# Kernel tuning notes

Measured on AMD Instinct MI355X. Metric: run time of the kernel, lower is better.

Reference implementation:

```python
import jax, jax.numpy as jnp
import numpy as np

R_EPOCHS = 150
R_LR = 0.1
LMDA = 0.005


def setup_inputs() -> dict:
    key = jax.random.key(0)
    k_img, k_u = jax.random.split(key)
    B, K, M2 = 2048, 1024, 1024  # batch, neurons, M**2 pixels
    img = jax.random.normal(k_img, (B, M2), dtype=jnp.float32)
    U = jax.random.normal(k_u, (K, M2), dtype=jnp.float32)
    U = U / jnp.linalg.norm(U, axis=1, keepdims=True)  # F.normalize(U, dim=1)
    return {"img": img, "U": U}


def _soft_threshold(x, alpha):
    # relu(x - a) - relu(-x - a) == sign(x) * max(|x| - a, 0)
    return jnp.sign(x) * jnp.maximum(jnp.abs(x) - alpha, 0.0)


def reference(img, U):
    B = img.shape[0]
    K = U.shape[0]

    def step(R, _):
        # dL/dR for L = sum((img - R @ U)**2)  ->  2 * (R @ U - img) @ U.T
        grad = 2.0 * ((R @ U - img) @ U.T)
        R = _soft_threshold(R - R_LR * grad, LMDA)
        return R, None

    R0 = jnp.zeros((B, K), dtype=img.dtype)
    R, _ = jax.lax.scan(step, R0, None, length=R_EPOCHS)
    # In torch, R is updated via .data / no_grad, so it is a leaf w.r.t. autograd
    R = jax.lax.stop_gradient(R)
    return R @ U
```

## Files before the change

kernel.cpp:

```cpp
#include <hip/hip_runtime.h>
#include <cstddef>
#include <cstdint>

using f32x4  = __attribute__((ext_vector_type(4))) float;
using bf16x8 = __attribute__((ext_vector_type(8))) short;
using u16x4  = __attribute__((ext_vector_type(4))) unsigned short;
using u32x4  = __attribute__((ext_vector_type(4))) unsigned int;
typedef unsigned short u16;
typedef unsigned int   u32;

#define LMDA 0.005f

__device__ __forceinline__ u16 f2bf(float f) {
    union { float f; uint32_t u; } v; v.f = f;
    return (u16)((v.u + 0x7FFFu + ((v.u >> 16) & 1u)) >> 16);
}
__device__ __forceinline__ float bf2f(u16 b) {
    union { uint32_t u; float f; } v; v.u = ((uint32_t)b) << 16;
    return v.f;
}
__device__ __forceinline__ float bits2f(u32 u) {
    union { uint32_t u; float f; } v; v.u = u;
    return v.f;
}
__device__ __forceinline__ void split2(float x, u16& h, u16& l) {
    h = f2bf(x); l = f2bf(x - bf2f(h));
}
__device__ __forceinline__ float sthr(float x) {
    float ax = fabsf(x) - LMDA;
    return ax > 0.0f ? copysignf(ax, x) : 0.0f;
}

__device__ __forceinline__ void gload16(const u16* g, u16* l) {
    __builtin_amdgcn_global_load_lds(
        (const __attribute__((address_space(1))) unsigned int*)(const void*)g,
        (__attribute__((address_space(3))) unsigned int*)(void*)l, 16, 0, 0);
}

__global__ __launch_bounds__(512, 2)
void pc_step(const u16* __restrict__ Rh, const u16* __restrict__ Rl,
             const u16* __restrict__ Woh, const u32* __restrict__ Cp,
             u16* __restrict__ Nh, u16* __restrict__ Nl)
{
    __shared__ __align__(16) u16 S[3][24 * 512];

    const int fid = blockIdx.x;
    const int sid = (fid & 7) * 32 + (fid >> 3);
    const int tr = sid >> 3;
    const int tc = sid & 7;
    const int row0 = tr << 6;
    const int col0 = tc << 7;

    const int tid  = threadIdx.x;
    const int lane = tid & 63;
    const int w    = tid >> 6;
    const int mr   = w >> 2;
    const int nc   = w & 3;
    const int l15  = lane & 15;
    const int lg   = lane >> 4;
    const int l8   = lane << 3;

    const u16* gsrc[3];
    int loff[3];
    #pragma unroll
    for (int t = 0; t < 3; ++t) {
        const int c = w * 3 + t;
        const u16* base;
        int r, kh;
        if (c < 8) {
            kh = (c >> 2) & 1;
            base = Rh;
            r = row0 + ((c & 3) << 4) + l15;
        } else {
            const int cb = c - 8;
            kh = cb >> 3;
            base = Woh;
            r = col0 + ((cb & 7) << 4) + l15;
        }
        gsrc[t] = base + ((size_t)r << 10) + (kh << 5) + (lg << 3);
        loff[t] = (c << 9) + l8;
    }
    auto stage = [&](int b, int k) {
        #pragma unroll
        for (int t = 0; t < 3; ++t)
            gload16(gsrc[t] + k, &S[b][loff[t]]);
    };

    f32x4 acc[2][2] = {};

    stage(0, 0);
    stage(1, 64);

    for (int s = 0; s < 16; ++s) {
        if (s < 15) asm volatile("s_waitcnt vmcnt(3)" ::: "memory");
        else        asm volatile("s_waitcnt vmcnt(0)" ::: "memory");
        __builtin_amdgcn_s_barrier();
        asm volatile("" ::: "memory");
        if (s + 2 < 16) {
            int nb = s + 2; nb -= (nb >= 3) ? 3 : 0; nb -= (nb >= 3) ? 3 : 0;
            nb = (s + 2) % 3;
            stage(nb, (s + 2) << 6);
        }

        const u16* Sb = S[s % 3];
        bf16x8 rh[2][2], wo[2][2];
        #pragma unroll
        for (int kh = 0; kh < 2; ++kh) {
            #pragma unroll
            for (int mf = 0; mf < 2; ++mf) {
                const int g = (mr << 1) + mf;
                rh[mf][kh] = *(const bf16x8*)&Sb[(((kh << 2) + g) << 9) + l8];
            }
            #pragma unroll
            for (int nf = 0; nf < 2; ++nf) {
                const int g = (nc << 1) + nf;
                wo[nf][kh] = *(const bf16x8*)&Sb[((8 + (kh << 3) + g) << 9) + l8];
            }
        }
        #pragma unroll
        for (int kh = 0; kh < 2; ++kh)
            #pragma unroll
            for (int mf = 0; mf < 2; ++mf)
                #pragma unroll
                for (int nf = 0; nf < 2; ++nf)
                    acc[mf][nf] = __builtin_amdgcn_mfma_f32_16x16x32_bf16(
                        wo[nf][kh], rh[mf][kh], acc[mf][nf], 0, 0, 0);
        asm volatile("" ::: "memory");
    }

    #pragma unroll
    for (int mf = 0; mf < 2; ++mf) {
        #pragma unroll
        for (int nf = 0; nf < 2; ++nf) {
            const int m  = row0 + (mr << 5) + (mf << 4) + l15;
            const int n0 = col0 + (nc << 5) + (nf << 4) + (lg << 2);
            const size_t idx = ((size_t)m << 10) + n0;
            const u16x4 rh4 = *(const u16x4*)&Rh[idx];
            const u16x4 rl4 = *(const u16x4*)&Rl[idx];
            const u32x4 cp4 = *(const u32x4*)&Cp[idx];
            u16x4 hv, lv;
            #pragma unroll
            for (int e = 0; e < 4; ++e) {
                const float cs = bits2f(cp4[e] & 0xFFFF0000u) + bits2f(cp4[e] << 16);
                float r = bf2f(rh4[e]) + bf2f(rl4[e]);
                float x = acc[mf][nf][e] + 0.8f * r + cs;
                u16 hh, ll; split2(sthr(x), hh, ll);
                hv[e] = hh; lv[e] = ll;
            }
            *(u16x4*)&Nh[idx] = hv;
            *(u16x4*)&Nl[idx] = lv;
        }
    }
}

__global__ __launch_bounds__(512, 2)
void gemm_fin(const u16* __restrict__ Rh, const u16* __restrict__ Rl,
              const u16* __restrict__ Bm, float* __restrict__ OutF)
{
    constexpr int NCH = 32;
    __shared__ __align__(16) u16 S[2][NCH * 512];

    const int fid = blockIdx.x;
    const int sid = (fid & 7) * 32 + (fid >> 3);
    const int tr = sid >> 3;
    const int tc = sid & 7;
    const int row0 = tr << 6;
    const int col0 = tc << 7;

    const int tid  = threadIdx.x;
    const int lane = tid & 63;
    const int w    = tid >> 6;
    const int mr   = w >> 2;
    const int nc   = w & 3;
    const int l15  = lane & 15;
    const int lg   = lane >> 4;
    const int l8   = lane << 3;

    const u16* gsrc[4];
    int loff[4];
    #pragma unroll
    for (int t = 0; t < 4; ++t) {
        const int c = (w << 2) + t;
        const u16* base;
        int r, kh;
        if (c < 16) {
            const int h = c >> 3;
            kh = (c >> 2) & 1;
            base = h ? Rl : Rh;
            r = row0 + ((c & 3) << 4) + l15;
        } else {
            const int cb = c - 16;
            kh = cb >> 3;
            base = Bm;
            r = col0 + ((cb & 7) << 4) + l15;
        }
        gsrc[t] = base + ((size_t)r << 10) + (kh << 5) + (lg << 3);
        loff[t] = (c << 9) + l8;
    }
    auto stage = [&](int b, int k) {
        #pragma unroll
        for (int t = 0; t < 4; ++t)
            gload16(gsrc[t] + k, &S[b][loff[t]]);
    };

    f32x4 acc[2][2] = {};

    stage(0, 0);

    for (int s = 0; s < 16; ++s) {
        asm volatile("s_waitcnt vmcnt(0)" ::: "memory");
        __builtin_amdgcn_s_barrier();
        asm volatile("" ::: "memory");
        if (s < 15) stage((s + 1) & 1, (s + 1) << 6);

        const u16* Sb = S[s & 1];
        bf16x8 rh[2][2], rl[2][2], wo[2][2];
        #pragma unroll
        for (int kh = 0; kh < 2; ++kh) {
            #pragma unroll
            for (int mf = 0; mf < 2; ++mf) {
                const int g = (mr << 1) + mf;
                rh[mf][kh] = *(const bf16x8*)&Sb[(((kh << 2) + g) << 9) + l8];
                rl[mf][kh] = *(const bf16x8*)&Sb[((8 + (kh << 2) + g) << 9) + l8];
            }
            #pragma unroll
            for (int nf = 0; nf < 2; ++nf) {
                const int g = (nc << 1) + nf;
                wo[nf][kh] = *(const bf16x8*)&Sb[((16 + (kh << 3) + g) << 9) + l8];
            }
        }
        #pragma unroll
        for (int kh = 0; kh < 2; ++kh)
            #pragma unroll
            for (int mf = 0; mf < 2; ++mf)
                #pragma unroll
                for (int nf = 0; nf < 2; ++nf) {
                    acc[mf][nf] = __builtin_amdgcn_mfma_f32_16x16x32_bf16(
                        wo[nf][kh], rh[mf][kh], acc[mf][nf], 0, 0, 0);
                    acc[mf][nf] = __builtin_amdgcn_mfma_f32_16x16x32_bf16(
                        wo[nf][kh], rl[mf][kh], acc[mf][nf], 0, 0, 0);
                }
        asm volatile("" ::: "memory");
    }

    #pragma unroll
    for (int mf = 0; mf < 2; ++mf)
        #pragma unroll
        for (int nf = 0; nf < 2; ++nf) {
            const int m  = row0 + (mr << 5) + (mf << 4) + l15;
            const int n0 = col0 + (nc << 5) + (nf << 4) + (lg << 2);
            *(f32x4*)&OutF[((size_t)m << 10) + n0] = acc[mf][nf];
        }
}

template<int EPI>
__global__ __launch_bounds__(512, 2)
void gemm_ista(const u16* __restrict__ Ah, const u16* __restrict__ Al,
               const u16* __restrict__ Bh, const u16* __restrict__ Bl,
               int Nt,
               u32* __restrict__ OutP,
               u16* __restrict__ OutH, u16* __restrict__ OutL)
{
    __shared__ __align__(16) u16 S[3][48 * 512];

    const int nwg = gridDim.x;
    const int fid = blockIdx.x;
    const int sid = (fid & 7) * (nwg >> 3) + (fid >> 3);
    const int row0 = (sid / Nt) << 7;
    const int col0 = (sid % Nt) << 6;

    const int tid  = threadIdx.x;
    const int lane = tid & 63;
    const int w    = tid >> 6;
    const int mr = w >> 2, nc = (w >> 1) & 1, ks = w & 1;

    const u16* gb[6];
    int cf[6];
    #pragma unroll
    for (int t = 0; t < 6; ++t) {
        const int c = w * 6 + t;
        const u16* base; int r; int kss;
        if (c < 32) {
            const int h = (c >> 4) & 1; kss = (c >> 3) & 1;
            base = h ? Al : Ah;
            r = row0 + ((c & 7) << 4) + (lane & 15);
        } else {
            const int cb = c - 32;
            const int h = (cb >> 3) & 1; kss = (cb >> 2) & 1;
            base = h ? Bl : Bh;
            r = col0 + ((cb & 3) << 4) + (lane & 15);
        }
        gb[t] = base + ((size_t)r << 10) + (kss << 5) + ((lane >> 4) << 3);
        cf[t] = c << 9;
    }
    auto stage = [&](int b, int koff) {
        #pragma unroll
        for (int t = 0; t < 6; ++t)
            gload16(gb[t] + koff, &S[b][cf[t]]);
    };

    f32x4 acc[4][2] = {};

    stage(0, 0);
    stage(1, 64);

    #pragma unroll
    for (int s = 0; s < 16; ++s) {
        if (s <= 14) asm volatile("s_waitcnt vmcnt(6)" ::: "memory");
        else         asm volatile("s_waitcnt vmcnt(0)" ::: "memory");
        __builtin_amdgcn_s_barrier();
        asm volatile("" ::: "memory");
        if (s + 2 < 16) stage((s + 2) % 3, (s + 2) << 6);

        const u16* Sb = S[s % 3];
        const int ab = (ks << 3) + (mr << 2);
        const int bb = 32 + (ks << 2) + (nc << 1);
        bf16x8 ah[4], al[4], bh[2], bl[2];
        #pragma unroll
        for (int i = 0; i < 4; ++i) {
            ah[i] = *(const bf16x8*)&Sb[(ab + i)      * 512 + (lane << 3)];
            al[i] = *(const bf16x8*)&Sb[(ab + 16 + i) * 512 + (lane << 3)];
        }
        #pragma unroll
        for (int j = 0; j < 2; ++j) {
            bh[j] = *(const bf16x8*)&Sb[(bb + j)     * 512 + (lane << 3)];
            bl[j] = *(const bf16x8*)&Sb[(bb + 8 + j) * 512 + (lane << 3)];
        }
        #pragma unroll
        for (int i = 0; i < 4; ++i)
            #pragma unroll
            for (int j = 0; j < 2; ++j)
                acc[i][j] = __builtin_amdgcn_mfma_f32_16x16x32_bf16(ah[i], bh[j], acc[i][j], 0, 0, 0);
        #pragma unroll
        for (int i = 0; i < 4; ++i)
            #pragma unroll
            for (int j = 0; j < 2; ++j)
                acc[i][j] = __builtin_amdgcn_mfma_f32_16x16x32_bf16(al[i], bh[j], acc[i][j], 0, 0, 0);
        #pragma unroll
        for (int i = 0; i < 4; ++i)
            #pragma unroll
            for (int j = 0; j < 2; ++j)
                acc[i][j] = __builtin_amdgcn_mfma_f32_16x16x32_bf16(ah[i], bl[j], acc[i][j], 0, 0, 0);
        asm volatile("" ::: "memory");
    }

    __syncthreads();
    f32x4* red = (f32x4*)&S[0][0];
    const int wquad = (mr << 1) + nc;
    #pragma unroll
    for (int ih = 0; ih < 2; ++ih) {
        #pragma unroll
        for (int j = 0; j < 2; ++j) {
            const int isrc = ks ? ih : (2 + ih);
            const int slot = ((((wquad << 1) | ks) << 2) | (ih << 1) | j);
            red[slot * 64 + lane] = acc[isrc][j];
        }
    }
    __syncthreads();

    const int gr0 = row0 + (mr << 6) + ((lane >> 4) << 2);
    const int gc  = col0 + (nc << 5) + (lane & 15);
    #pragma unroll
    for (int ih = 0; ih < 2; ++ih) {
        #pragma unroll
        for (int j = 0; j < 2; ++j) {
            const int i    = ks ? (2 + ih) : ih;
            const int slot = ((((wquad << 1) | (ks ^ 1)) << 2) | (ih << 1) | j);
            f32x4 sum = acc[i][j] + red[slot * 64 + lane];
            #pragma unroll
            for (int e = 0; e < 4; ++e) {
                const int grow = gr0 + (i << 4) + e;
                const int gcol = gc + (j << 4);
                const size_t idx = ((size_t)grow << 10) + gcol;
                const float p = sum[e];
                if (EPI == 1) {
                    float f = 0.2f * p;
                    u16 ch, cl; split2(f, ch, cl);
                    OutP[idx] = (((u32)ch) << 16) | (u32)cl;
                    u16 h, l; split2(sthr(f), h, l);
                    OutH[idx] = h; OutL[idx] = l;
                } else {
                    float x = (grow == gcol) ? 0.0f : -0.2f * p;
                    OutH[idx] = f2bf(x);
                }
            }
        }
    }
}

__global__ void k_split(const float* __restrict__ in, u16* __restrict__ hi,
                        u16* __restrict__ lo, int n)
{
    int i = blockIdx.x * 256 + threadIdx.x;
    if (i < n) { u16 h, l; split2(in[i], h, l); hi[i] = h; lo[i] = l; }
}

__global__ __launch_bounds__(256)
void k_transpose_split(const float* __restrict__ in, u16* __restrict__ hi,
                       u16* __restrict__ lo)
{
    __shared__ float t[32][33];
    const int bx = blockIdx.x, by = blockIdx.y;
    const int lx = threadIdx.x & 31, ly = threadIdx.x >> 5;
    #pragma unroll
    for (int rr = 0; rr < 4; ++rr) {
        int r = ly * 4 + rr;
        t[r][lx] = in[(size_t)(by * 32 + r) * 1024 + bx * 32 + lx];
    }
    __syncthreads();
    #pragma unroll
    for (int rr = 0; rr < 4; ++rr) {
        int r = ly * 4 + rr;
        u16 h, l; split2(t[lx][r], h, l);
        size_t idx = (size_t)(bx * 32 + r) * 1024 + by * 32 + lx;
        hi[idx] = h; lo[idx] = l;
    }
}

extern "C" void kernel_launch(void* const* d_in, const int* in_sizes, int n_in,
                              void* d_out, int out_size, void* d_ws, size_t ws_size,
                              hipStream_t stream) {
    const float* img = (const float*)d_in[0];
    const float* U   = (const float*)d_in[1];
    float* out = (float*)d_out;

    char* ws = (char*)d_ws;
    auto MB = [](size_t m) { return m << 20; };
    u16*   Uh  = (u16*)(ws + MB(0));
    u16*   Ul  = (u16*)(ws + MB(2));
    u16*   Uth = (u16*)(ws + MB(4));
    u16*   Utl = (u16*)(ws + MB(6));
    u16*   Woh = (u16*)(ws + MB(8));
    u32*   Cp  = (u32*)(ws + MB(12));
    u16*   Rah = (u16*)(ws + MB(20));
    u16*   Ral = (u16*)(ws + MB(24));
    u16*   Rbh = (u16*)(ws + MB(28));
    u16*   Rbl = (u16*)(ws + MB(32));
    u16*   Ih  = Rbh;
    u16*   Il  = Rbl;

    k_split<<<4096, 256, 0, stream>>>(U, Uh, Ul, 1024 * 1024);
    k_split<<<8192, 256, 0, stream>>>(img, Ih, Il, 2048 * 1024);
    k_transpose_split<<<dim3(32, 32), 256, 0, stream>>>(U, Uth, Utl);

    gemm_ista<4><<<128, 512, 0, stream>>>(Uh, Ul, Uh, Ul, 16,
                                          nullptr, Woh, nullptr);
    gemm_ista<1><<<256, 512, 0, stream>>>(Ih, Il, Uh, Ul, 16,
                                          Cp, Rah, Ral);

    u16 *ch = Rah, *cl = Ral, *nh = Rbh, *nl = Rbl;
    for (int it = 0; it < 149; ++it) {
        pc_step<<<256, 512, 0, stream>>>(ch, cl, Woh, Cp, nh, nl);
        u16* t;
        t = ch; ch = nh; nh = t;
        t = cl; cl = nl; nl = t;
    }

    gemm_fin<<<256, 512, 0, stream>>>(ch, cl, Uth, out);
}
```

Measured before the change: 2.691 ms.

## Restructure pc_step to 4-wave blocks with 32-wide K stages and 2x4 MFMA tiles

The per-iteration ISTA step kernel drops from 8 to 4 waves per block. Each wave now computes a 32x64 output sub-tile (2x4 MFMA fragments) instead of 32x32, and the K loop runs 32 stages of 32 instead of 16 stages of 64. Shared memory per block halves, so more blocks can be resident. The intent is to raise register-level reuse of the loaded fragments and improve occupancy. In exchange there are twice as many barriers and pipeline stages per tile, and fewer waves share each block's loads.

```diff
diff --git a/kernel.cpp b/kernel.cpp
--- a/kernel.cpp
+++ b/kernel.cpp
@@ -37,12 +37,12 @@
         (__attribute__((address_space(3))) unsigned int*)(void*)l, 16, 0, 0);
 }
 
-__global__ __launch_bounds__(512, 2)
+__global__ __launch_bounds__(256, 4)
 void pc_step(const u16* __restrict__ Rh, const u16* __restrict__ Rl,
              const u16* __restrict__ Woh, const u32* __restrict__ Cp,
              u16* __restrict__ Nh, u16* __restrict__ Nl)
 {
-    __shared__ __align__(16) u16 S[3][24 * 512];
+    __shared__ __align__(16) u16 S[3][12 * 512];
 
     const int fid = blockIdx.x;
     const int sid = (fid & 7) * 32 + (fid >> 3);
@@ -54,8 +54,8 @@
     const int tid  = threadIdx.x;
     const int lane = tid & 63;
     const int w    = tid >> 6;
-    const int mr   = w >> 2;
-    const int nc   = w & 3;
+    const int mr   = w >> 1;
+    const int nc   = w & 1;
     const int l15  = lane & 15;
     const int lg   = lane >> 4;
     const int l8   = lane << 3;
@@ -66,18 +66,10 @@
     for (int t = 0; t < 3; ++t) {
         const int c = w * 3 + t;
         const u16* base;
-        int r, kh;
-        if (c < 8) {
-            kh = (c >> 2) & 1;
-            base = Rh;
-            r = row0 + ((c & 3) << 4) + l15;
-        } else {
-            const int cb = c - 8;
-            kh = cb >> 3;
-            base = Woh;
-            r = col0 + ((cb & 7) << 4) + l15;
-        }
-        gsrc[t] = base + ((size_t)r << 10) + (kh << 5) + (lg << 3);
+        int r;
+        if (c < 4) { base = Rh;  r = row0 + ((c & 3) << 4) + l15; }
+        else       { base = Woh; r = col0 + ((c - 4) << 4) + l15; }
+        gsrc[t] = base + ((size_t)r << 10) + (lg << 3);
         loff[t] = (c << 9) + l8;
     }
     auto stage = [&](int b, int k) {
@@ -86,54 +78,41 @@
             gload16(gsrc[t] + k, &S[b][loff[t]]);
     };
 
-    f32x4 acc[2][2] = {};
+    f32x4 acc[2][4] = {};
 
     stage(0, 0);
-    stage(1, 64);
-
-    for (int s = 0; s < 16; ++s) {
-        if (s < 15) asm volatile("s_waitcnt vmcnt(3)" ::: "memory");
+    stage(1, 32);
+
+    for (int s = 0; s < 32; ++s) {
+        if (s < 31) asm volatile("s_waitcnt vmcnt(3)" ::: "memory");
         else        asm volatile("s_waitcnt vmcnt(0)" ::: "memory");
         __builtin_amdgcn_s_barrier();
         asm volatile("" ::: "memory");
-        if (s + 2 < 16) {
-            int nb = s + 2; nb -= (nb >= 3) ? 3 : 0; nb -= (nb >= 3) ? 3 : 0;
-            nb = (s + 2) % 3;
-            stage(nb, (s + 2) << 6);
-        }
+        if (s + 2 < 32) stage((s + 2) % 3, (s + 2) << 5);
 
         const u16* Sb = S[s % 3];
-        bf16x8 rh[2][2], wo[2][2];
-        #pragma unroll
-        for (int kh = 0; kh < 2; ++kh) {
-            #pragma unroll
-            for (int mf = 0; mf < 2; ++mf) {
-                const int g = (mr << 1) + mf;
-                rh[mf][kh] = *(const bf16x8*)&Sb[(((kh << 2) + g) << 9) + l8];
-            }
-            #pragma unroll
-            for (int nf = 0; nf < 2; ++nf) {
-                const int g = (nc << 1) + nf;
-                wo[nf][kh] = *(const bf16x8*)&Sb[((8 + (kh << 3) + g) << 9) + l8];
-            }
-        }
-        #pragma unroll
-        for (int kh = 0; kh < 2; ++kh)
-            #pragma unroll
-            for (int mf = 0; mf < 2; ++mf)
-                #pragma unroll
-                for (int nf = 0; nf < 2; ++nf)
-                    acc[mf][nf] = __builtin_amdgcn_mfma_f32_16x16x32_bf16(
-                        wo[nf][kh], rh[mf][kh], acc[mf][nf], 0, 0, 0);
+        bf16x8 rh[2], wo[4];
+        #pragma unroll
+        for (int mf = 0; mf < 2; ++mf)
+            rh[mf] = *(const bf16x8*)&Sb[(((mr << 1) + mf) << 9) + l8];
+        #pragma unroll
+        for (int nf = 0; nf < 4; ++nf)
+            wo[nf] = *(const bf16x8*)&Sb[((4 + (nc << 2) + nf) << 9) + l8];
+        #pragma unroll
+        for (int mf = 0; mf < 2; ++mf)
+            #pragma unroll
+            for (int nf = 0; nf < 4; ++nf)
+                acc[mf][nf] = __builtin_amdgcn_mfma_f32_16x16x32_bf16(
+                    wo[nf], rh[mf], acc[mf][nf], 0, 0, 0);
         asm volatile("" ::: "memory");
     }
 
     #pragma unroll
     for (int mf = 0; mf < 2; ++mf) {
         #pragma unroll
-        for (int nf = 0; nf < 2; ++nf) {
+        for (int nf = 0; nf < 4; ++nf) {
             const int m  = row0 + (mr << 5) + (mf << 4) + l15;
-            const int n0 = col0 + (nc << 5) + (nf << 4) + (lg << 2);
+            const int n0 = col0 + (nc << 6) + (nf << 4) + (lg << 2);
             const size_t idx = ((size_t)m << 10) + n0;
             const u16x4 rh4 = *(const u16x4*)&Rh[idx];
             const u16x4 rl4 = *(const u16x4*)&Rl[idx];
@@ -450,7 +429,7 @@
 
     u16 *ch = Rah, *cl = Ral, *nh = Rbh, *nl = Rbl;
     for (int it = 0; it < 149; ++it) {
-        pc_step<<<256, 512, 0, stream>>>(ch, cl, Woh, Cp, nh, nl);
+        pc_step<<<256, 256, 0, stream>>>(ch, cl, Woh, Cp, nh, nl);
         u16* t;
         t = ch; ch = nh; nh = t;
         t = cl; cl = nl; nl = t;
```

New measurement: 2.766 ms. 2.8% more time.

## Replace LDS-staged ISTA step with register-prefetched global loads and smaller tiles

Applied to the files above, without the earlier changes.

The per-iteration ISTA step kernel no longer stages R and W tiles through shared memory with barriers. Each wave now loads its MFMA fragments straight from global memory into a three-deep register ring, prefetching two k-steps ahead. Tiles shrink to 32x128 and blocks to 256 threads, which doubles the grid to 512 blocks. This removes LDS traffic and barrier stalls, but each wave re-reads the shared R rows from global memory or cache, raising L2 traffic and register pressure.

```diff
diff --git a/kernel.cpp b/kernel.cpp
--- a/kernel.cpp
+++ b/kernel.cpp
@@ -37,84 +37,63 @@
         (__attribute__((address_space(3))) unsigned int*)(void*)l, 16, 0, 0);
 }
 
-__global__ __launch_bounds__(512, 2)
-void pc_step(const u16* __restrict__ Rh, const u16* __restrict__ Rl,
-             const u16* __restrict__ Woh, const u32* __restrict__ Cp,
-             u16* __restrict__ Nh, u16* __restrict__ Nl)
+__global__ __launch_bounds__(256, 2)
+void pc_reg(const u16* __restrict__ Rh, const u16* __restrict__ Rl,
+            const u16* __restrict__ Woh, const u32* __restrict__ Cp,
+            u16* __restrict__ Nh, u16* __restrict__ Nl)
 {
-    __shared__ __align__(16) u16 S[3][24 * 512];
-
     const int fid = blockIdx.x;
-    const int sid = (fid & 7) * 32 + (fid >> 3);
+    const int sid = (fid & 7) * 64 + (fid >> 3);
     const int tr = sid >> 3;
     const int tc = sid & 7;
-    const int row0 = tr << 6;
+    const int row0 = tr << 5;
     const int col0 = tc << 7;
 
     const int tid  = threadIdx.x;
     const int lane = tid & 63;
-    const int w    = tid >> 6;
-    const int mr   = w >> 2;
-    const int nc   = w & 3;
+    const int nc   = tid >> 6;
     const int l15  = lane & 15;
     const int lg   = lane >> 4;
-    const int l8   = lane << 3;
-
-    const u16* gsrc[3];
-    int loff[3];
-    #pragma unroll
-    for (int t = 0; t < 3; ++t) {
-        const int c = w * 3 + t;
-        const u16* base;
-        int r, kh;
-        if (c < 8) {
-            kh = (c >> 2) & 1;
-            base = Rh;
-            r = row0 + ((c & 3) << 4) + l15;
-        } else {
-            const int cb = c - 8;
-            kh = cb >> 3;
-            base = Woh;
-            r = col0 + ((cb & 7) << 4) + l15;
-        }
-        gsrc[t] = base + ((size_t)r << 10) + (kh << 5) + (lg << 3);
-        loff[t] = (c << 9) + l8;
-    }
-    auto stage = [&](int b, int k) {
-        #pragma unroll
-        for (int t = 0; t < 3; ++t)
-            gload16(gsrc[t] + k, &S[b][loff[t]]);
-    };
+
+    const u16* rbase[2];
+    const u16* wbase[2];
+    #pragma unroll
+    for (int mf = 0; mf < 2; ++mf)
+        rbase[mf] = Rh + (((size_t)(row0 + (mf << 4) + l15)) << 10) + (lg << 3);
+    #pragma unroll
+    for (int nf = 0; nf < 2; ++nf)
+        wbase[nf] = Woh + (((size_t)(col0 + (nc << 5) + (nf << 4) + l15)) << 10) + (lg << 3);
 
     f32x4 acc[2][2] = {};
 
-    stage(0, 0);
-    stage(1, 64);
-
+    bf16x8 rf[3][2][2], wf[3][2][2];
+
+    #pragma unroll
+    for (int p = 0; p < 2; ++p) {
+        #pragma unroll
+        for (int kh = 0; kh < 2; ++kh) {
+            #pragma unroll
+            for (int mf = 0; mf < 2; ++mf)
+                rf[p][mf][kh] = *(const bf16x8*)(rbase[mf] + (p << 6) + (kh << 5));
+            #pragma unroll
+            for (int nf = 0; nf < 2; ++nf)
+                wf[p][nf][kh] = *(const bf16x8*)(wbase[nf] + (p << 6) + (kh << 5));
+        }
+    }
+
+    #pragma unroll
     for (int s = 0; s < 16; ++s) {
-        if (s < 15) asm volatile("s_waitcnt vmcnt(3)" ::: "memory");
-        else        asm volatile("s_waitcnt vmcnt(0)" ::: "memory");
-        __builtin_amdgcn_s_barrier();
-        asm volatile("" ::: "memory");
+        const int cur = s % 3;
+        const int nxt = (s + 2) % 3;
         if (s + 2 < 16) {
-            int nb = s + 2; nb -= (nb >= 3) ? 3 : 0; nb -= (nb >= 3) ? 3 : 0;
-            nb = (s + 2) % 3;
-            stage(nb, (s + 2) << 6);
-        }
-
-        const u16* Sb = S[s % 3];
-        bf16x8 rh[2][2], wo[2][2];
-        #pragma unroll
-        for (int kh = 0; kh < 2; ++kh) {
-            #pragma unroll
-            for (int mf = 0; mf < 2; ++mf) {
-                const int g = (mr << 1) + mf;
-                rh[mf][kh] = *(const bf16x8*)&Sb[(((kh << 2) + g) << 9) + l8];
-            }
-            #pragma unroll
-            for (int nf = 0; nf < 2; ++nf) {
-                const int g = (nc << 1) + nf;
-                wo[nf][kh] = *(const bf16x8*)&Sb[((8 + (kh << 3) + g) << 9) + l8];
+            #pragma unroll
+            for (int kh = 0; kh < 2; ++kh) {
+                #pragma unroll
+                for (int mf = 0; mf < 2; ++mf)
+                    rf[nxt][mf][kh] = *(const bf16x8*)(rbase[mf] + ((s + 2) << 6) + (kh << 5));
+                #pragma unroll
+                for (int nf = 0; nf < 2; ++nf)
+                    wf[nxt][nf][kh] = *(const bf16x8*)(wbase[nf] + ((s + 2) << 6) + (kh << 5));
             }
         }
         #pragma unroll
@@ -124,15 +103,14 @@
                 #pragma unroll
                 for (int nf = 0; nf < 2; ++nf)
                     acc[mf][nf] = __builtin_amdgcn_mfma_f32_16x16x32_bf16(
-                        wo[nf][kh], rh[mf][kh], acc[mf][nf], 0, 0, 0);
-        asm volatile("" ::: "memory");
+                        wf[cur][nf][kh], rf[cur][mf][kh], acc[mf][nf], 0, 0, 0);
     }
 
     #pragma unroll
     for (int mf = 0; mf < 2; ++mf) {
         #pragma unroll
         for (int nf = 0; nf < 2; ++nf) {
-            const int m  = row0 + (mr << 5) + (mf << 4) + l15;
+            const int m  = row0 + (mf << 4) + l15;
             const int n0 = col0 + (nc << 5) + (nf << 4) + (lg << 2);
             const size_t idx = ((size_t)m << 10) + n0;
             const u16x4 rh4 = *(const u16x4*)&Rh[idx];
@@ -220,13 +198,13 @@
             #pragma unroll
             for (int mf = 0; mf < 2; ++mf) {
                 const int g = (mr << 1) + mf;
-                rh[mf][kh] = *(const bf16x8*)&Sb[(((kh << 2) + g) << 9) + l8];
-                rl[mf][kh] = *(const bf16x8*)&Sb[((8 + (kh << 2) + g) << 9) + l8];
+                rh[mf][kh] = *(const bf16x8*)&S[s & 1][(((kh << 2) + g) << 9) + l8];
+                rl[mf][kh] = *(const bf16x8*)&S[s & 1][((8 + (kh << 2) + g) << 9) + l8];
             }
             #pragma unroll
             for (int nf = 0; nf < 2; ++nf) {
                 const int g = (nc << 1) + nf;
-                wo[nf][kh] = *(const bf16x8*)&Sb[((16 + (kh << 3) + g) << 9) + l8];
+                wo[nf][kh] = *(const bf16x8*)&S[s & 1][((16 + (kh << 3) + g) << 9) + l8];
             }
         }
         #pragma unroll
@@ -241,6 +219,7 @@
                         wo[nf][kh], rl[mf][kh], acc[mf][nf], 0, 0, 0);
                 }
         asm volatile("" ::: "memory");
+        (void)Sb;
     }
 
     #pragma unroll
@@ -450,7 +429,7 @@
 
     u16 *ch = Rah, *cl = Ral, *nh = Rbh, *nl = Rbl;
     for (int it = 0; it < 149; ++it) {
-        pc_step<<<256, 512, 0, stream>>>(ch, cl, Woh, Cp, nh, nl);
+        pc_reg<<<512, 256, 0, stream>>>(ch, cl, Woh, Cp, nh, nl);
         u16* t;
         t = ch; ch = nh; nh = t;
         t = cl; cl = nl; nl = t;
```

Result: slower. 5.134 ms (+90.8%).
